# Kernel optimization log

Hardware: AMD Instinct MI355X
Metric: run time of the kernel (lower is better)

Reference implementation:

```python
import jax, jax.numpy as jnp
import numpy as np
from jax import lax

D_MODEL, D_STATE, D_CONV, EXPAND = 1024, 16, 4, 2
D_INNER = D_MODEL * EXPAND
BATCH, SEQ = 4, 2048


def setup_inputs() -> dict:
    key = jax.random.key(0)
    ks = jax.random.split(key, 9)
    s = lambda fan_in: 1.0 / np.sqrt(fan_in)
    return {
        "x": jax.random.normal(ks[0], (BATCH, SEQ, D_MODEL), dtype=jnp.float32),
        "W_in": jax.random.normal(ks[1], (D_MODEL, 2 * D_INNER), dtype=jnp.float32) * s(D_MODEL),
        "conv_w": jax.random.normal(ks[2], (D_INNER, 1, D_CONV), dtype=jnp.float32) * s(D_CONV),
        "conv_b": jax.random.normal(ks[3], (D_INNER,), dtype=jnp.float32) * 0.01,
        "W_x": jax.random.normal(ks[4], (D_INNER, 2 * D_STATE), dtype=jnp.float32) * s(D_INNER),
        "W_dt": jax.random.normal(ks[5], (D_INNER, D_INNER), dtype=jnp.float32) * s(D_INNER),
        "b_dt": jax.random.normal(ks[6], (D_INNER,), dtype=jnp.float32) * 0.01,
        "A_log": jnp.log(jnp.arange(1, D_STATE + 1, dtype=jnp.float32)),
        "D": jnp.ones((D_INNER,), dtype=jnp.float32),
        "W_out": jax.random.normal(ks[7], (D_INNER, D_MODEL), dtype=jnp.float32) * s(D_INNER),
    }


def _mamba_forward(x, W_in, conv_w, conv_b, W_x, W_dt, b_dt, A_log, D, W_out):
    batch, seq_len, _ = x.shape
    xz = x @ W_in                                   # (B,L,2*Di)
    x_in, z = jnp.split(xz, 2, axis=-1)
    # causal depthwise conv1d: pad (d_conv-1) on the left == pad both sides then slice [:L]
    x_c = lax.conv_general_dilated(
        x_in.transpose(0, 2, 1), conv_w,
        window_strides=(1,), padding=[(D_CONV - 1, 0)],
        feature_group_count=D_INNER,
        dimension_numbers=("NCH", "OIH", "NCH"),
    ) + conv_b[None, :, None]
    x_conv = jax.nn.silu(x_c.transpose(0, 2, 1))    # (B,L,Di)

    A = -jnp.exp(A_log)                             # (N,)
    Bm, Cm = jnp.split(x_conv @ W_x, 2, axis=-1)    # each (B,L,N)
    dt = jax.nn.softplus(x_conv @ W_dt + b_dt)      # (B,L,Di)

    def step(h, ins):
        u_t, dt_t, B_t, C_t = ins                   # (B,Di),(B,Di),(B,N),(B,N)
        dA = jnp.exp(dt_t[:, :, None] * A)          # (B,Di,N)
        h = dA * h + (dt_t * u_t)[:, :, None] * B_t[:, None, :]
        y_t = jnp.einsum("bdn,bn->bd", h, C_t)
        return h, y_t

    h0 = jnp.zeros((batch, D_INNER, D_STATE), dtype=x.dtype)
    xs = (x_conv.transpose(1, 0, 2), dt.transpose(1, 0, 2),
          Bm.transpose(1, 0, 2), Cm.transpose(1, 0, 2))
    _, ys = lax.scan(step, h0, xs)                  # ys: (L,B,Di)
    y = ys.transpose(1, 0, 2)

    y = y + x_conv * D
    y = y * jax.nn.silu(z)
    return y @ W_out


def reference(x, W_in, conv_w, conv_b, W_x, W_dt, b_dt, A_log, D, W_out):
    return _mamba_forward(x, W_in, conv_w, conv_b, W_x, W_dt, b_dt, A_log, D, W_out)
```

## Files before the change

kernel.cpp:

```cpp
#include <hip/hip_runtime.h>

#define DM     1024
#define DI     2048
#define DST    16
#define NBATCH 4
#define SEQ    2048
#define MROWS  (NBATCH*SEQ)
#define NCHUNK 16
#define CLEN   (SEQ/NCHUNK)

typedef unsigned short u16;
typedef unsigned int   u32;
typedef unsigned long long u64;

typedef __bf16 bf16x8 __attribute__((ext_vector_type(8)));
typedef float  f32x4  __attribute__((ext_vector_type(4)));

typedef const __attribute__((address_space(1))) u32* gas_ptr;
typedef __attribute__((address_space(3))) u32* las_ptr;
#define GLOAD16(g, l) __builtin_amdgcn_global_load_lds((gas_ptr)(g), (las_ptr)(l), 16, 0, 0)
#define MFMA16(a, b, c) __builtin_amdgcn_mfma_f32_16x16x32_bf16((a), (b), (c), 0, 0, 0)

static __device__ __forceinline__ u16 f2bf(float f) {
  u32 u = __builtin_bit_cast(u32, f);
  u = (u + 0x7FFFu + ((u >> 16) & 1u)) >> 16;
  return (u16)u;
}
static __device__ __forceinline__ float bf2f(u16 h) {
  return __builtin_bit_cast(float, (u32)h << 16);
}
static __device__ __forceinline__ float sigmoid_f(float x) {
  return __builtin_amdgcn_rcpf(1.f + __expf(-x));
}

__global__ __launch_bounds__(256)
void split_cast_k(const float* __restrict__ in, u16* __restrict__ hi,
                  u16* __restrict__ lo, int n4) {
  const int i = blockIdx.x * 256 + threadIdx.x;
  if (i >= n4) return;
  const float4 v = reinterpret_cast<const float4*>(in)[i];
  u16 h0 = f2bf(v.x), h1 = f2bf(v.y), h2 = f2bf(v.z), h3 = f2bf(v.w);
  u16 l0 = f2bf(v.x - bf2f(h0)), l1 = f2bf(v.y - bf2f(h1));
  u16 l2 = f2bf(v.z - bf2f(h2)), l3 = f2bf(v.w - bf2f(h3));
  reinterpret_cast<u64*>(hi)[i] = (u64)h0 | ((u64)h1<<16) | ((u64)h2<<32) | ((u64)h3<<48);
  reinterpret_cast<u64*>(lo)[i] = (u64)l0 | ((u64)l1<<16) | ((u64)l2<<32) | ((u64)l3<<48);
}

template<int SPLIT>
__global__ __launch_bounds__(256)
void transpose_cast_k(const float* __restrict__ in, u16* __restrict__ hi,
                      u16* __restrict__ lo, int R, int C) {
  __shared__ float tile[32][33];
  const int c0 = blockIdx.x * 32, r0 = blockIdx.y * 32;
  const int tx = threadIdx.x, ty = threadIdx.y;
  #pragma unroll
  for (int i = ty; i < 32; i += 8)
    tile[i][tx] = in[(size_t)(r0 + i) * C + c0 + tx];
  __syncthreads();
  #pragma unroll
  for (int i = ty; i < 32; i += 8) {
    const float v = tile[tx][i];
    const u16 h = f2bf(v);
    hi[(size_t)(c0 + i) * R + r0 + tx] = h;
    if (SPLIT) lo[(size_t)(c0 + i) * R + r0 + tx] = f2bf(v - bf2f(h));
  }
}

template<int EPI>
__global__ __launch_bounds__(512, 2)
void gemm8_k(const u16* __restrict__ Ah, const u16* __restrict__ Al,
             const u16* __restrict__ Bh, const u16* __restrict__ Bl,
             void* __restrict__ O1, u16* __restrict__ O2,
             const float* __restrict__ bias,
             int M, int N, int K, int nmt) {
  __shared__ __align__(16) u16 lds[8 * 8192];
  const int tid  = threadIdx.x;
  const int lane = tid & 63;
  const int wid  = tid >> 6;
  const int wr = wid >> 2, wc = wid & 3;

  const int nwg = gridDim.x;
  const int wg  = (blockIdx.x & 7) * (nwg >> 3) + (blockIdx.x >> 3);
  const int bm  = (wg % nmt) * 256;
  const int bn  = (wg / nmt) * 256;

  const bool three = (EPI == 1) && (bn < DI);
  const int KH = K >> 5;

  f32x4 acc[8][4];
  #pragma unroll
  for (int m = 0; m < 8; ++m)
    #pragma unroll
    for (int n = 0; n < 4; ++n)
      #pragma unroll
      for (int r = 0; r < 4; ++r) acc[m][n][r] = 0.f;

  auto stA = [&](const u16* __restrict__ src, int kh, int slot) {
    const int kb = kh << 5;
    #pragma unroll
    for (int q = 0; q < 2; ++q) {
      const int bch = (q * 8 + wid) * 64;
      const int L = bch + lane;
      const int r = L >> 2;
      const int c = (L & 3) ^ ((r >> 1) & 3);
      GLOAD16(src + (size_t)(bm + r) * K + kb + c * 8, lds + slot * 8192 + bch * 8);
    }
  };
  auto stB = [&](const u16* __restrict__ src, int kh, int slot) {
    const int kb = kh << 5;
    #pragma unroll
    for (int q = 0; q < 2; ++q) {
      const int bch = (q * 8 + wid) * 64;
      const int L = bch + lane;
      const int r = L >> 2;
      const int c = (L & 3) ^ ((r >> 1) & 3);
      GLOAD16(src + (size_t)(bn + r) * K + kb + c * 8, lds + 32768 + slot * 8192 + bch * 8);
    }
  };
  const int fr = lane & 15, fc = lane >> 4;
  bf16x8 afr[4], bfr[4];
  auto rdAm = [&](int slot, int mb) {
    #pragma unroll
    for (int m = 0; m < 4; ++m) {
      const int r = wr * 128 + (mb + m) * 16 + fr;
      afr[m] = *reinterpret_cast<const bf16x8*>(&lds[slot * 8192 + (r * 4 + (fc ^ ((r >> 1) & 3))) * 8]);
    }
  };
  auto rdBn = [&](int slot) {
    #pragma unroll
    for (int n = 0; n < 4; ++n) {
      const int r = wc * 64 + n * 16 + fr;
      bfr[n] = *reinterpret_cast<const bf16x8*>(&lds[32768 + slot * 8192 + (r * 4 + (fc ^ ((r >> 1) & 3))) * 8]);
    }
  };
  auto MF = [&](int mb) {
    __builtin_amdgcn_s_barrier();
    __builtin_amdgcn_s_setprio(1);
    #pragma unroll
    for (int m = 0; m < 4; ++m)
      #pragma unroll
      for (int n = 0; n < 4; ++n)
        acc[mb + m][n] = MFMA16(afr[m], bfr[n], acc[mb + m][n]);
    __builtin_amdgcn_s_setprio(0);
    __builtin_amdgcn_s_barrier();
  };

  if (EPI == 0 || (EPI == 1 && !three)) {
    stA(Ah, 0, 0); stB(Bh, 0, 0);
    stA(Ah, 1, 1); stB(Bh, 1, 1);
    stA(Ah, 2, 2); stB(Bh, 2, 2);
    asm volatile("s_waitcnt vmcnt(8)" ::: "memory");
    __builtin_amdgcn_s_barrier();
    for (int k = 0; k < KH; ++k) {
      const int s = k & 3;
      rdBn(s); rdAm(s, 0);
      if (k + 3 < KH) stA(Ah, k + 3, (k + 3) & 3);
      MF(0);
      rdAm(s, 4);
      if (k + 3 < KH) { stB(Bh, k + 3, (k + 3) & 3);
                        asm volatile("s_waitcnt vmcnt(4)" ::: "memory"); }
      else            { asm volatile("s_waitcnt vmcnt(0)" ::: "memory"); }
      MF(4);
    }
  } else if (EPI == 2) {
    stA(Ah, 0, 0); stB(Bh, 0, 0); stB(Bl, 0, 1);
    stA(Ah, 1, 1); stB(Bh, 1, 2); stB(Bl, 1, 3);
    asm volatile("s_waitcnt vmcnt(6)" ::: "memory");
    __builtin_amdgcn_s_barrier();
    for (int k = 0; k < KH; ++k) {
      const int sa = k & 3, sbh = (2 * k) & 3, sbl = (2 * k + 1) & 3;
      rdBn(sbh); rdAm(sa, 0);
      if (k + 2 < KH) stA(Ah, k + 2, (k + 2) & 3);
      MF(0);
      rdAm(sa, 4);
      MF(4);
      rdBn(sbl); rdAm(sa, 0);
      if (k + 2 < KH) stB(Bh, k + 2, sbh);
      MF(0);
      rdAm(sa, 4);
      if (k + 2 < KH) { stB(Bl, k + 2, sbl);
                        asm volatile("s_waitcnt vmcnt(6)" ::: "memory"); }
      else            { asm volatile("s_waitcnt vmcnt(0)" ::: "memory"); }
      MF(4);
    }
  } else {
    stA(Ah, 0, 0); stB(Bl, 0, 0); stB(Bh, 0, 1); stA(Al, 0, 1);
    stA(Ah, 1, 2); stB(Bl, 1, 2); stB(Bh, 1, 3);
    asm volatile("s_waitcnt vmcnt(6)" ::: "memory");
    __builtin_amdgcn_s_barrier();
    for (int k = 0; k < KH; ++k) {
      const int sah = (2 * k) & 3, sal = (2 * k + 1) & 3;
      const int sbl = (2 * k) & 3, sbh = (2 * k + 1) & 3;
      rdBn(sbl); rdAm(sah, 0);
      if (k + 1 < KH) stA(Al, k + 1, (2 * k + 3) & 3);
      MF(0);
      rdAm(sah, 4);
      MF(4);
      rdBn(sbh); rdAm(sah, 0);
      if (k + 2 < KH) stB(Bl, k + 2, sbl);
      MF(0);
      rdAm(sah, 4);
      MF(4);
      rdAm(sal, 0);
      if (k + 2 < KH) stA(Ah, k + 2, sah);
      MF(0);
      rdAm(sal, 4);
      if (k + 2 < KH) { stB(Bh, k + 2, sbh);
                        asm volatile("s_waitcnt vmcnt(6)" ::: "memory"); }
      else            { asm volatile("s_waitcnt vmcnt(0)" ::: "memory"); }
      MF(4);
    }
  }

  const int rr = fc * 4;
  #pragma unroll
  for (int m = 0; m < 8; ++m) {
    #pragma unroll
    for (int n = 0; n < 4; ++n) {
      const int gr0 = bm + wr * 128 + m * 16 + rr;
      const int gc  = bn + wc * 64 + n * 16 + fr;
      #pragma unroll
      for (int r = 0; r < 4; ++r) {
        float v = acc[m][n][r];
        const int gr = gr0 + r;
        if (EPI == 0) {
          ((float*)O1)[(size_t)gr * N + gc] = v;
        } else if (EPI == 1) {
          if (gc < DI) ((u16*)O1)[(size_t)gr * DI + gc] = f2bf(v);
          else         O2[(size_t)gr * DI + gc - DI] = f2bf(v);
        } else {
          v += bias[gc];
          v = (v > 20.f) ? v : __logf(1.f + __expf(v));
          const u16 h = f2bf(v);
          ((u16*)O1)[(size_t)gr * DI + gc] = h;
          O2[(size_t)gr * DI + gc] = f2bf(v - bf2f(h));
        }
      }
    }
  }
}

__global__ __launch_bounds__(256)
void gemm_bc2_k(const u16* __restrict__ A, const u16* __restrict__ BhT,
                const u16* __restrict__ BlT, float* __restrict__ BC) {
  const int lane = threadIdx.x & 63, wv = threadIdx.x >> 6;
  const int bm = blockIdx.x * 128 + wv * 32;
  const int fr = lane & 15, kc = lane >> 4;
  f32x4 acc[2][2];
  #pragma unroll
  for (int m = 0; m < 2; ++m)
    #pragma unroll
    for (int n = 0; n < 2; ++n)
      #pragma unroll
      for (int r = 0; r < 4; ++r) acc[m][n][r] = 0.f;
  for (int kk = 0; kk < DI / 32; ++kk) {
    const int k = kk * 32 + kc * 8;
    bf16x8 a[2], bh[2], bl[2];
    #pragma unroll
    for (int m = 0; m < 2; ++m)
      a[m] = *reinterpret_cast<const bf16x8*>(&A[(size_t)(bm + m*16 + fr) * DI + k]);
    #pragma unroll
    for (int n = 0; n < 2; ++n) {
      bh[n] = *reinterpret_cast<const bf16x8*>(&BhT[(size_t)(n*16 + fr) * DI + k]);
      bl[n] = *reinterpret_cast<const bf16x8*>(&BlT[(size_t)(n*16 + fr) * DI + k]);
    }
    #pragma unroll
    for (int m = 0; m < 2; ++m)
      #pragma unroll
      for (int n = 0; n < 2; ++n) {
        acc[m][n] = MFMA16(a[m], bh[n], acc[m][n]);
        acc[m][n] = MFMA16(a[m], bl[n], acc[m][n]);
      }
  }
  #pragma unroll
  for (int m = 0; m < 2; ++m)
    #pragma unroll
    for (int n = 0; n < 2; ++n)
      #pragma unroll
      for (int r = 0; r < 4; ++r)
        BC[(size_t)(bm + m*16 + kc*4 + r) * 32 + n*16 + fr] = acc[m][n][r];
}

__global__ __launch_bounds__(256)
void conv_silu_k(const u16* __restrict__ xin, const float* __restrict__ cw,
                 const float* __restrict__ cb, u16* __restrict__ xc) {
  const int idx = blockIdx.x * 256 + threadIdx.x;
  const int d = idx & (DI - 1);
  const int row = idx >> 11;
  const int l = row & (SEQ - 1);
  const int bb = row >> 11;
  float acc = cb[d];
  #pragma unroll
  for (int i = 0; i < 4; ++i) {
    const int ls = l + i - 3;
    if (ls >= 0)
      acc = fmaf(bf2f(xin[(size_t)(bb * SEQ + ls) * DI + d]), cw[d*4 + i], acc);
  }
  const float s = acc * sigmoid_f(acc);
  xc[idx] = f2bf(s);
}

__global__ __launch_bounds__(256)
void scan1_k(const u16* __restrict__ dtH, const u16* __restrict__ dtL,
             const u16* __restrict__ u, const float* __restrict__ BC,
             float* __restrict__ Pb, float* __restrict__ Sb) {
  const int blk = blockIdx.x;
  const int db = blk & 7;
  const int c  = (blk >> 3) & (NCHUNK - 1);
  const int bb = blk >> 7;
  const int d  = db * 256 + threadIdx.x;
  float P[DST], S[DST];
  #pragma unroll
  for (int n = 0; n < DST; ++n) { P[n] = 1.f; S[n] = 0.f; }
  for (int s = 0; s < CLEN; ++s) {
    const size_t row = (size_t)bb * SEQ + c * CLEN + s;
    const float dtv = bf2f(dtH[row * DI + d]) + bf2f(dtL[row * DI + d]);
    const float uv  = bf2f(u[row * DI + d]);
    const float dtu = dtv * uv;
    const float* Brow = &BC[row * 32];
    const float q = __expf(-dtv);
    float a = 1.f;
    #pragma unroll
    for (int n = 0; n < DST; ++n) {
      a *= q;
      P[n] *= a;
      S[n] = fmaf(a, S[n], dtu * Brow[n]);
    }
  }
  const size_t off = ((size_t)(bb * NCHUNK + c) * DI + d) * DST;
  #pragma unroll
  for (int n = 0; n < DST; ++n) { Pb[off + n] = P[n]; Sb[off + n] = S[n]; }
}

__global__ __launch_bounds__(256)
void scan2_k(const float* __restrict__ Pb, const float* __restrict__ Sb,
             float* __restrict__ hs) {
  const int idx = blockIdx.x * 256 + threadIdx.x;
  const int n = idx & (DST - 1);
  const int d = (idx >> 4) & (DI - 1);
  const int bb = idx >> 15;
  float h = 0.f;
  #pragma unroll
  for (int c = 0; c < NCHUNK; ++c) {
    const size_t off = ((size_t)(bb * NCHUNK + c) * DI + d) * DST + n;
    hs[off] = h;
    h = fmaf(Pb[off], h, Sb[off]);
  }
}

__global__ __launch_bounds__(256)
void scan3_k(const u16* __restrict__ dtH, const u16* __restrict__ dtL,
             u16* uy, const float* __restrict__ BC,
             const float* __restrict__ hs, const float* __restrict__ Dv) {
  const int blk = blockIdx.x;
  const int db = blk & 7;
  const int c  = (blk >> 3) & (NCHUNK - 1);
  const int bb = blk >> 7;
  const int d  = db * 256 + threadIdx.x;
  const float Dd = Dv[d];
  float h[DST];
  const size_t hoff = ((size_t)(bb * NCHUNK + c) * DI + d) * DST;
  #pragma unroll
  for (int n = 0; n < DST; ++n) h[n] = hs[hoff + n];
  for (int s = 0; s < CLEN; ++s) {
    const size_t row = (size_t)bb * SEQ + c * CLEN + s;
    const float dtv = bf2f(dtH[row * DI + d]) + bf2f(dtL[row * DI + d]);
    const float uv  = bf2f(uy[row * DI + d]);
    const float dtu = dtv * uv;
    const float* Brow = &BC[row * 32];
    const float q = __expf(-dtv);
    float a = 1.f;
    float yv = uv * Dd;
    #pragma unroll
    for (int n = 0; n < DST; ++n) {
      a *= q;
      h[n] = fmaf(a, h[n], dtu * Brow[n]);
      yv = fmaf(h[n], Brow[DST + n], yv);
    }
    uy[row * DI + d] = f2bf(yv);
  }
}

__global__ __launch_bounds__(256)
void elemwise_k(u16* g_io, const u16* __restrict__ z) {
  const int idx = blockIdx.x * 256 + threadIdx.x;
  const float zf = bf2f(z[idx]);
  float v = bf2f(g_io[idx]) * zf * sigmoid_f(zf);
  g_io[idx] = f2bf(v);
}

extern "C" void kernel_launch(void* const* d_in, const int* in_sizes, int n_in,
                              void* d_out, int out_size, void* d_ws, size_t ws_size,
                              hipStream_t stream) {
  (void)in_sizes; (void)n_in;
  const float* x      = (const float*)d_in[0];
  const float* W_in   = (const float*)d_in[1];
  const float* conv_w = (const float*)d_in[2];
  const float* conv_b = (const float*)d_in[3];
  const float* W_x    = (const float*)d_in[4];
  const float* W_dt   = (const float*)d_in[5];
  const float* b_dt   = (const float*)d_in[6];
  const float* A_log  = (const float*)d_in[7];  (void)A_log;
  const float* Dvec   = (const float*)d_in[8];
  const float* W_out  = (const float*)d_in[9];
  float* out = (float*)d_out;

  char* w = (char*)d_ws;
  size_t used = 0;
  auto alloc = [&](size_t bytes) {
    char* p = w + used; used += (bytes + 255) & ~(size_t)255; return p;
  };
  u16* x_h    = (u16*)alloc((size_t)MROWS * DM * 2);
  u16* x_l    = (u16*)alloc((size_t)MROWS * DM * 2);
  u16* WinT_h = (u16*)alloc((size_t)(2*DI) * DM * 2);
  u16* WinT_l = (u16*)alloc((size_t)(2*DI) * DM * 2);
  u16* WdtT_h = (u16*)alloc((size_t)DI * DI * 2);
  u16* WdtT_l = (u16*)alloc((size_t)DI * DI * 2);
  u16* WxT_h  = (u16*)alloc((size_t)32 * DI * 2);
  u16* WxT_l  = (u16*)alloc((size_t)32 * DI * 2);
  u16* xin    = (u16*)alloc((size_t)MROWS * DI * 2);
  u16* z_bf   = (u16*)alloc((size_t)MROWS * DI * 2);
  u16* xc     = (u16*)alloc((size_t)MROWS * DI * 2);
  u16* dt_h   = (u16*)alloc((size_t)MROWS * DI * 2);
  const size_t NEED = used;
  u16* dt_l = xin;
  char* xr = (char*)x_h;
  float* Pb    = (float*)(xr);
  float* Sb    = (float*)(xr + 8388608);
  float* hsb   = (float*)(xr + 2 * 8388608);
  float* BC    = (float*)(xr + 3 * 8388608);
  u16*   WoutT = (u16*)  (xr + 3 * 8388608 + 1048576);

  if (ws_size < NEED) {
    hipMemsetAsync(d_out, 0, (size_t)out_size * 4, stream);
    return;
  }

  split_cast_k<<<(MROWS*DM/4 + 255)/256, 256, 0, stream>>>(x, x_h, x_l, MROWS*DM/4);
  transpose_cast_k<1><<<dim3((2*DI)/32, DM/32), dim3(32,8), 0, stream>>>(W_in, WinT_h, WinT_l, DM, 2*DI);
  transpose_cast_k<1><<<dim3(DI/32, DI/32), dim3(32,8), 0, stream>>>(W_dt, WdtT_h, WdtT_l, DI, DI);
  transpose_cast_k<1><<<dim3(1, DI/32), dim3(32,8), 0, stream>>>(W_x, WxT_h, WxT_l, DI, 32);

  gemm8_k<1><<<512, 512, 0, stream>>>(x_h, x_l, WinT_h, WinT_l,
                                      xin, z_bf, nullptr, MROWS, 2*DI, DM, 32);

  conv_silu_k<<<MROWS*DI/256, 256, 0, stream>>>(xin, conv_w, conv_b, xc);

  transpose_cast_k<0><<<dim3(DM/32, DI/32), dim3(32,8), 0, stream>>>(W_out, WoutT, nullptr, DI, DM);

  gemm_bc2_k<<<MROWS/128, 256, 0, stream>>>(xc, WxT_h, WxT_l, BC);

  gemm8_k<2><<<256, 512, 0, stream>>>(xc, nullptr, WdtT_h, WdtT_l,
                                      dt_h, dt_l, b_dt, MROWS, DI, DI, 32);

  scan1_k<<<NBATCH*NCHUNK*(DI/256), 256, 0, stream>>>(dt_h, dt_l, xc, BC, Pb, Sb);
  scan2_k<<<NBATCH*DI*DST/256,      256, 0, stream>>>(Pb, Sb, hsb);
  scan3_k<<<NBATCH*NCHUNK*(DI/256), 256, 0, stream>>>(dt_h, dt_l, xc, BC, hsb, Dvec);

  elemwise_k<<<MROWS*DI/256, 256, 0, stream>>>(xc, z_bf);

  gemm8_k<0><<<128, 512, 0, stream>>>(xc, nullptr, WoutT, nullptr,
                                      out, nullptr, nullptr, MROWS, DM, DI, 32);
}
```

Before: 751.3 us.

## Store dt as fp32, hoist GEMM address math, remap workgroups, relax vmcnt

The dt GEMM epilogue now writes one fp32 value per element instead of a bf16 hi/lo pair, and both scan kernels read that fp32 buffer directly. The dt buffer reuses the adjacent xin and dtx allocations, which are reordered so the space is contiguous. The GEMM also precomputes its global and LDS addresses once instead of per K-step, and maps workgroups in chunks of 256. Its pipelined wait now allows more outstanding loads (vmcnt 8 instead of 4), which risks overlapping an in-flight load with the LDS slot being read.

```diff
diff --git a/kernel.cpp b/kernel.cpp
--- a/kernel.cpp
+++ b/kernel.cpp
@@ -80,7 +80,11 @@
   const int wr = wid >> 2, wc = wid & 3;
 
   const int nwg = gridDim.x;
-  const int wg  = (blockIdx.x & 7) * (nwg >> 3) + (blockIdx.x >> 3);
+  const int b   = blockIdx.x;
+  const int chunk = b >> 8;
+  const int inner = b & 255;
+  const int ni  = (nwg < 256) ? nwg : 256;
+  const int wg  = chunk * 256 + (inner & 7) * (ni >> 3) + (inner >> 3);
   const int bm  = (wg % nmt) * 256;
   const int bn  = (wg / nmt) * 256;
 
@@ -95,43 +99,53 @@
       #pragma unroll
       for (int r = 0; r < 4; ++r) acc[m][n][r] = 0.f;
 
+  size_t gA[2], gB[2];
+  u32 lst[2];
+  #pragma unroll
+  for (int q = 0; q < 2; ++q) {
+    const int bch = (q * 8 + wid) * 64;
+    const int L = bch + lane;
+    const int r = L >> 2;
+    const int c = (L & 3) ^ ((r >> 1) & 3);
+    gA[q] = (size_t)(bm + r) * K + c * 8;
+    gB[q] = (size_t)(bn + r) * K + c * 8;
+    lst[q] = bch * 8;
+  }
+  const int fr = lane & 15, fc = lane >> 4;
+  u32 offA[8], offB[4];
+  #pragma unroll
+  for (int m = 0; m < 8; ++m) {
+    const int r = wr * 128 + m * 16 + fr;
+    offA[m] = (r * 4 + (fc ^ ((r >> 1) & 3))) * 8;
+  }
+  #pragma unroll
+  for (int n = 0; n < 4; ++n) {
+    const int r = wc * 64 + n * 16 + fr;
+    offB[n] = (r * 4 + (fc ^ ((r >> 1) & 3))) * 8;
+  }
+
   auto stA = [&](const u16* __restrict__ src, int kh, int slot) {
     const int kb = kh << 5;
     #pragma unroll
-    for (int q = 0; q < 2; ++q) {
-      const int bch = (q * 8 + wid) * 64;
-      const int L = bch + lane;
-      const int r = L >> 2;
-      const int c = (L & 3) ^ ((r >> 1) & 3);
-      GLOAD16(src + (size_t)(bm + r) * K + kb + c * 8, lds + slot * 8192 + bch * 8);
-    }
+    for (int q = 0; q < 2; ++q)
+      GLOAD16(src + gA[q] + kb, lds + slot * 8192 + lst[q]);
   };
   auto stB = [&](const u16* __restrict__ src, int kh, int slot) {
     const int kb = kh << 5;
     #pragma unroll
-    for (int q = 0; q < 2; ++q) {
-      const int bch = (q * 8 + wid) * 64;
-      const int L = bch + lane;
-      const int r = L >> 2;
-      const int c = (L & 3) ^ ((r >> 1) & 3);
-      GLOAD16(src + (size_t)(bn + r) * K + kb + c * 8, lds + 32768 + slot * 8192 + bch * 8);
-    }
-  };
-  const int fr = lane & 15, fc = lane >> 4;
+    for (int q = 0; q < 2; ++q)
+      GLOAD16(src + gB[q] + kb, lds + 32768 + slot * 8192 + lst[q]);
+  };
   bf16x8 afr[4], bfr[4];
   auto rdAm = [&](int slot, int mb) {
     #pragma unroll
-    for (int m = 0; m < 4; ++m) {
-      const int r = wr * 128 + (mb + m) * 16 + fr;
-      afr[m] = *reinterpret_cast<const bf16x8*>(&lds[slot * 8192 + (r * 4 + (fc ^ ((r >> 1) & 3))) * 8]);
-    }
+    for (int m = 0; m < 4; ++m)
+      afr[m] = *reinterpret_cast<const bf16x8*>(&lds[slot * 8192 + offA[mb + m]]);
   };
   auto rdBn = [&](int slot) {
     #pragma unroll
-    for (int n = 0; n < 4; ++n) {
-      const int r = wc * 64 + n * 16 + fr;
-      bfr[n] = *reinterpret_cast<const bf16x8*>(&lds[32768 + slot * 8192 + (r * 4 + (fc ^ ((r >> 1) & 3))) * 8]);
-    }
+    for (int n = 0; n < 4; ++n)
+      bfr[n] = *reinterpret_cast<const bf16x8*>(&lds[32768 + slot * 8192 + offB[n]]);
   };
   auto MF = [&](int mb) {
     __builtin_amdgcn_s_barrier();
@@ -158,7 +172,7 @@
       MF(0);
       rdAm(s, 4);
       if (k + 3 < KH) { stB(Bh, k + 3, (k + 3) & 3);
-                        asm volatile("s_waitcnt vmcnt(4)" ::: "memory"); }
+                        asm volatile("s_waitcnt vmcnt(8)" ::: "memory"); }
       else            { asm volatile("s_waitcnt vmcnt(0)" ::: "memory"); }
       MF(4);
     }
@@ -231,9 +245,7 @@
         } else {
           v += bias[gc];
           v = (v > 20.f) ? v : __logf(1.f + __expf(v));
-          const u16 h = f2bf(v);
-          ((u16*)O1)[(size_t)gr * DI + gc] = h;
-          O2[(size_t)gr * DI + gc] = f2bf(v - bf2f(h));
+          ((float*)O1)[(size_t)gr * DI + gc] = v;
         }
       }
     }
@@ -301,9 +313,9 @@
 }
 
 __global__ __launch_bounds__(256)
-void scan1_k(const u16* __restrict__ dtH, const u16* __restrict__ dtL,
-             const u16* __restrict__ u, const float* __restrict__ BC,
-             float* __restrict__ Pb, float* __restrict__ Sb) {
+void scan1_k(const float* __restrict__ dt, const u16* __restrict__ u,
+             const float* __restrict__ BC, float* __restrict__ Pb,
+             float* __restrict__ Sb) {
   const int blk = blockIdx.x;
   const int db = blk & 7;
   const int c  = (blk >> 3) & (NCHUNK - 1);
@@ -314,7 +326,7 @@
   for (int n = 0; n < DST; ++n) { P[n] = 1.f; S[n] = 0.f; }
   for (int s = 0; s < CLEN; ++s) {
     const size_t row = (size_t)bb * SEQ + c * CLEN + s;
-    const float dtv = bf2f(dtH[row * DI + d]) + bf2f(dtL[row * DI + d]);
+    const float dtv = dt[row * DI + d];
     const float uv  = bf2f(u[row * DI + d]);
     const float dtu = dtv * uv;
     const float* Brow = &BC[row * 32];
@@ -349,9 +361,9 @@
 }
 
 __global__ __launch_bounds__(256)
-void scan3_k(const u16* __restrict__ dtH, const u16* __restrict__ dtL,
-             u16* uy, const float* __restrict__ BC,
-             const float* __restrict__ hs, const float* __restrict__ Dv) {
+void scan3_k(const float* __restrict__ dt, u16* uy,
+             const float* __restrict__ BC, const float* __restrict__ hs,
+             const float* __restrict__ Dv) {
   const int blk = blockIdx.x;
   const int db = blk & 7;
   const int c  = (blk >> 3) & (NCHUNK - 1);
@@ -364,7 +376,7 @@
   for (int n = 0; n < DST; ++n) h[n] = hs[hoff + n];
   for (int s = 0; s < CLEN; ++s) {
     const size_t row = (size_t)bb * SEQ + c * CLEN + s;
-    const float dtv = bf2f(dtH[row * DI + d]) + bf2f(dtL[row * DI + d]);
+    const float dtv = dt[row * DI + d];
     const float uv  = bf2f(uy[row * DI + d]);
     const float dtu = dtv * uv;
     const float* Brow = &BC[row * 32];
@@ -418,12 +430,13 @@
   u16* WdtT_l = (u16*)alloc((size_t)DI * DI * 2);
   u16* WxT_h  = (u16*)alloc((size_t)32 * DI * 2);
   u16* WxT_l  = (u16*)alloc((size_t)32 * DI * 2);
-  u16* xin    = (u16*)alloc((size_t)MROWS * DI * 2);
   u16* z_bf   = (u16*)alloc((size_t)MROWS * DI * 2);
   u16* xc     = (u16*)alloc((size_t)MROWS * DI * 2);
-  u16* dt_h   = (u16*)alloc((size_t)MROWS * DI * 2);
+  u16* xin    = (u16*)alloc((size_t)MROWS * DI * 2);
+  char* dtx   = (char*)alloc((size_t)MROWS * DI * 2);
   const size_t NEED = used;
-  u16* dt_l = xin;
+  float* dtb = (float*)xin;
+  (void)dtx;
   char* xr = (char*)x_h;
   float* Pb    = (float*)(xr);
   float* Sb    = (float*)(xr + 8388608);
@@ -451,11 +464,11 @@
   gemm_bc2_k<<<MROWS/128, 256, 0, stream>>>(xc, WxT_h, WxT_l, BC);
 
   gemm8_k<2><<<256, 512, 0, stream>>>(xc, nullptr, WdtT_h, WdtT_l,
-                                      dt_h, dt_l, b_dt, MROWS, DI, DI, 32);
-
-  scan1_k<<<NBATCH*NCHUNK*(DI/256), 256, 0, stream>>>(dt_h, dt_l, xc, BC, Pb, Sb);
+                                      dtb, nullptr, b_dt, MROWS, DI, DI, 32);
+
+  scan1_k<<<NBATCH*NCHUNK*(DI/256), 256, 0, stream>>>(dtb, xc, BC, Pb, Sb);
   scan2_k<<<NBATCH*DI*DST/256,      256, 0, stream>>>(Pb, Sb, hsb);
-  scan3_k<<<NBATCH*NCHUNK*(DI/256), 256, 0, stream>>>(dt_h, dt_l, xc, BC, hsb, Dvec);
+  scan3_k<<<NBATCH*NCHUNK*(DI/256), 256, 0, stream>>>(dtb, xc, BC, hsb, Dvec);
 
   elemwise_k<<<MROWS*DI/256, 256, 0, stream>>>(xc, z_bf);
 
```

Result: faster. 704.7 us (-6.2%).
